# Kernel tuning notes

Hardware: AMD Instinct MI355X
Metric: run time of the kernel (lower is better)

Reference implementation:

```python
import jax, jax.numpy as jnp
import numpy as np

D_MODEL = 1024
H = 16
D_K = D_MODEL // H

def setup_inputs() -> dict:
    key = jax.random.key(0)
    ks = jax.random.split(key, 7)
    B, S = 4, 2048
    q = jax.random.normal(ks[0], (B, S, D_MODEL), dtype=jnp.float32)
    k = jax.random.normal(ks[1], (B, S, D_MODEL), dtype=jnp.float32)
    v = jax.random.normal(ks[2], (B, S, D_MODEL), dtype=jnp.float32)
    scale = 1.0 / np.sqrt(D_MODEL)
    w_q = jax.random.normal(ks[3], (D_MODEL, D_MODEL), dtype=jnp.float32) * scale
    w_k = jax.random.normal(ks[4], (D_MODEL, D_MODEL), dtype=jnp.float32) * scale
    w_v = jax.random.normal(ks[5], (D_MODEL, D_MODEL), dtype=jnp.float32) * scale
    w_o = jax.random.normal(ks[6], (D_MODEL, D_MODEL), dtype=jnp.float32) * scale
    return {"q": q, "k": k, "v": v, "w_q": w_q, "w_k": w_k, "w_v": w_v, "w_o": w_o}

def reference(q, k, v, w_q, w_k, w_v, w_o):
    B, S, _ = q.shape
    # Linear layers (no bias): x @ W^T, weights stored torch-style [out, in]
    def proj(x, w):
        y = jnp.einsum('bsd,ed->bse', x, w)
        return y.reshape(B, -1, H, D_K).transpose(0, 2, 1, 3)  # [B,H,S,d_k]
    query = proj(q, w_q)
    key_ = proj(k, w_k)
    value = proj(v, w_v)
    scores = jnp.einsum('bhqd,bhkd->bhqk', query, key_) / jnp.sqrt(jnp.float32(D_K))
    attn = jax.nn.softmax(scores, axis=-1)  # dropout p=0 -> identity
    x = jnp.einsum('bhqk,bhkd->bhqd', attn, value)
    x = x.transpose(0, 2, 1, 3).reshape(B, S, H * D_K)
    return jnp.einsum('bsd,ed->bse', x, w_o)
```

## Files before the change

### kernel.cpp

```cpp
#include <hip/hip_runtime.h>

typedef unsigned short ushort_t;
typedef __attribute__((ext_vector_type(8))) short bf16x8;
typedef __attribute__((ext_vector_type(4))) float f32x4;
typedef __attribute__((ext_vector_type(16))) float f32x16;
typedef __attribute__((ext_vector_type(4))) unsigned short ushort4v;
typedef __attribute__((ext_vector_type(4))) unsigned int uint4v;

__device__ __forceinline__ ushort_t f2bf(float f) {
  unsigned u = __float_as_uint(f);
  u += 0x7FFFu + ((u >> 16) & 1u);
  return (ushort_t)(u >> 16);
}

__device__ __forceinline__ unsigned cvt_pk(float lo, float hi) {
  unsigned r;
  asm("v_cvt_pk_bf16_f32 %0, %1, %2" : "=v"(r) : "v"(lo), "v"(hi));
  return r;
}

__device__ __forceinline__ float fast_exp2(float x) {
  float r;
  asm("v_exp_f32 %0, %1" : "=v"(r) : "v"(x));
  return r;
}

__device__ __forceinline__ void gload16(ushort_t* lds, const ushort_t* g) {
  __builtin_amdgcn_global_load_lds(
      (const __attribute__((address_space(1))) unsigned int*)g,
      (__attribute__((address_space(3))) unsigned int*)lds, 16, 0, 0);
}

__global__ void cast_w4(const float* __restrict__ s0, const float* __restrict__ s1,
                        const float* __restrict__ s2, const float* __restrict__ s3,
                        ushort_t* __restrict__ dst, int n4) {
  int i = blockIdx.x * blockDim.x + threadIdx.x;
  if (i >= n4) return;
  int z = blockIdx.y;
  const float* s = (z == 0) ? s0 : (z == 1) ? s1 : (z == 2) ? s2 : s3;
  float4 f = ((const float4*)s)[i];
  ushort4v o;
  o.x = f2bf(f.x); o.y = f2bf(f.y); o.z = f2bf(f.z); o.w = f2bf(f.w);
  ((ushort4v*)(dst + (size_t)z * n4 * 4))[i] = o;
}

template <int MODE, bool AF32>
__global__ __launch_bounds__(256, 2)
void gemm_bt(const void* __restrict__ Ap, const ushort_t* __restrict__ B,
             void* __restrict__ Cp, int M, int N, int K, float scale) {
  __shared__ __align__(16) ushort_t As[128 * 64];
  __shared__ __align__(16) ushort_t Bs[128 * 64];
  const int tid = threadIdx.x;
  const int wave = tid >> 6, lane = tid & 63;
  const int wr = wave >> 1, wc = wave & 1;
  const int frow = lane & 15, g = lane >> 4;
  const int r8 = lane >> 3, c8 = lane & 7;
  const int m0 = blockIdx.x * 128, n0 = blockIdx.y * 128;

  f32x4 acc[4][4] = {};

  const int sc = (c8 ^ r8) << 3;
  const ushort_t* Bb = B + (size_t)(n0 + wave * 32 + r8) * K + sc;
  ushort_t* AsW = &As[(wave * 32) * 64];
  ushort_t* BsW = &Bs[(wave * 32) * 64];

  const float* Af = nullptr;
  const ushort_t* Ab = nullptr;
  float a_pre[32];
  if constexpr (AF32) {
    Af = (const float*)Ap + (size_t)(m0 + wave * 32 + r8) * K + sc;
#pragma unroll
    for (int j = 0; j < 4; ++j) {
      *(float4*)&a_pre[j * 8]     = *(const float4*)(Af + (size_t)j * 8 * K);
      *(float4*)&a_pre[j * 8 + 4] = *(const float4*)(Af + (size_t)j * 8 * K + 4);
    }
  } else {
    Ab = (const ushort_t*)Ap + (size_t)(m0 + wave * 32 + r8) * K + sc;
  }

  for (int kt = 0; kt < K; kt += 64) {
    __syncthreads();
    if constexpr (AF32) {
#pragma unroll
      for (int j = 0; j < 4; ++j) {
        uint4v w;
        w[0] = cvt_pk(a_pre[j * 8 + 0], a_pre[j * 8 + 1]);
        w[1] = cvt_pk(a_pre[j * 8 + 2], a_pre[j * 8 + 3]);
        w[2] = cvt_pk(a_pre[j * 8 + 4], a_pre[j * 8 + 5]);
        w[3] = cvt_pk(a_pre[j * 8 + 6], a_pre[j * 8 + 7]);
        *(uint4v*)&AsW[j * 8 * 64 + lane * 8] = w;
        gload16(BsW + j * 8 * 64, Bb + (size_t)j * 8 * K + kt);
      }
    } else {
#pragma unroll
      for (int j = 0; j < 4; ++j) {
        gload16(AsW + j * 8 * 64, Ab + (size_t)j * 8 * K + kt);
        gload16(BsW + j * 8 * 64, Bb + (size_t)j * 8 * K + kt);
      }
    }
    __syncthreads();

    if constexpr (AF32) {
      if (kt + 64 < K) {
#pragma unroll
        for (int j = 0; j < 4; ++j) {
          *(float4*)&a_pre[j * 8]     = *(const float4*)(Af + (size_t)j * 8 * K + kt + 64);
          *(float4*)&a_pre[j * 8 + 4] = *(const float4*)(Af + (size_t)j * 8 * K + kt + 68);
        }
      }
    }

    bf16x8 af[4][2], bfr[4][2];
#pragma unroll
    for (int mi = 0; mi < 4; ++mi) {
      int row = wr * 64 + mi * 16 + frow;
#pragma unroll
      for (int ki = 0; ki < 2; ++ki)
        af[mi][ki] = *(const bf16x8*)&As[row * 64 + (((ki * 4 + g) ^ (row & 7)) << 3)];
    }
#pragma unroll
    for (int nf = 0; nf < 4; ++nf) {
      int row = wc * 64 + nf * 16 + frow;
#pragma unroll
      for (int ki = 0; ki < 2; ++ki)
        bfr[nf][ki] = *(const bf16x8*)&Bs[row * 64 + (((ki * 4 + g) ^ (row & 7)) << 3)];
    }
#pragma unroll
    for (int ki = 0; ki < 2; ++ki)
#pragma unroll
      for (int mi = 0; mi < 4; ++mi)
#pragma unroll
        for (int nf = 0; nf < 4; ++nf)
          acc[mi][nf] = __builtin_amdgcn_mfma_f32_16x16x32_bf16(
              af[mi][ki], bfr[nf][ki], acc[mi][nf], 0, 0, 0);
  }

#pragma unroll
  for (int mi = 0; mi < 4; ++mi)
#pragma unroll
    for (int nf = 0; nf < 4; ++nf)
#pragma unroll
      for (int r = 0; r < 4; ++r) {
        int m = m0 + wr * 64 + mi * 16 + g * 4 + r;
        int n = n0 + wc * 64 + nf * 16 + frow;
        float v = acc[mi][nf][r] * scale;
        if (MODE == 0) {
          ((ushort_t*)Cp)[(size_t)m * N + n] = f2bf(v);
        } else if (MODE == 1) {
          int b = m >> 11, s = m & 2047, h = n >> 6, dk = n & 63;
          ((ushort_t*)Cp)[(((size_t)((b * 16 + h) * 64 + dk)) << 11) + s] = f2bf(v);
        } else {
          ((float*)Cp)[(size_t)m * N + n] = v;
        }
      }
}

__global__ __launch_bounds__(256, 2)
void attn_kernel(const ushort_t* __restrict__ Qp, const ushort_t* __restrict__ Kp,
                 const ushort_t* __restrict__ Vt, ushort_t* __restrict__ Xb) {
  __shared__ __align__(16) ushort_t Ks[2][64 * 64];
  __shared__ __align__(16) ushort_t Vs[2][64 * 64];

  const int tid = threadIdx.x;
  const int wave = tid >> 6, lane = tid & 63;
  const int l31 = lane & 31, h = lane >> 5;
  const int f8 = lane >> 3, c8 = lane & 7;

  const int d = blockIdx.x;
  const int bh = ((d >> 6) << 3) | (d & 7);
  const int qt = (d >> 3) & 7;
  const int b = bh >> 4, hd = bh & 15;
  const int q0 = qt * 256 + wave * 64;

  bf16x8 qf[2][4];
  {
    const ushort_t* qb_ = Qp + (size_t)(b * 2048 + q0 + l31) * 1024 + hd * 64 + 8 * h;
#pragma unroll
    for (int qb = 0; qb < 2; ++qb)
#pragma unroll
      for (int ki = 0; ki < 4; ++ki)
        qf[qb][ki] = *(const bf16x8*)(qb_ + (size_t)(qb * 32) * 1024 + 16 * ki);
  }

  f32x16 oacc[2][2] = {};
  float ls[2][4] = {};

  const ushort_t* Kbase = Kp + (size_t)(b * 2048) * 1024 + hd * 64;
  const ushort_t* Vbase = Vt + ((size_t)(bh * 64) << 11);

  auto stage = [&](int kt, int sel) {
#pragma unroll
    for (int j = 0; j < 2; ++j) {
      int row = wave * 16 + j * 8 + f8;
      gload16(&Ks[sel][(wave * 16 + j * 8) * 64],
              Kbase + (size_t)(kt * 64 + row) * 1024 + ((c8 ^ f8) << 3));
      gload16(&Vs[sel][(wave * 16 + j * 8) * 64],
              Vbase + ((size_t)row << 11) + kt * 64 + ((c8 ^ f8) << 3));
    }
  };

  stage(0, 0);

  for (int kt = 0; kt < 32; ++kt) {
    const int cur = kt & 1;
    __syncthreads();
    if (kt < 31) stage(kt + 1, cur ^ 1);

    bf16x8 kf[2][4];
#pragma unroll
    for (int c = 0; c < 2; ++c)
#pragma unroll
      for (int ki = 0; ki < 4; ++ki) {
        int row = c * 32 + l31;
        kf[c][ki] = *(const bf16x8*)&Ks[cur][row * 64 + (((2 * ki + h) ^ (row & 7)) << 3)];
      }
    bf16x8 vf[4][2];
#pragma unroll
    for (int kc = 0; kc < 4; ++kc)
#pragma unroll
      for (int db = 0; db < 2; ++db) {
        int row = db * 32 + l31;
        vf[kc][db] = *(const bf16x8*)&Vs[cur][row * 64 + (((2 * kc + h) ^ (row & 7)) << 3)];
      }

#pragma unroll
    for (int qb = 0; qb < 2; ++qb) {
      f32x16 sacc[2];
      __builtin_amdgcn_s_setprio(1);
#pragma unroll
      for (int c = 0; c < 2; ++c) {
        sacc[c] = __builtin_amdgcn_mfma_f32_32x32x16_bf16(
            kf[c][0], qf[qb][0], (f32x16)(0.0f), 0, 0, 0);
#pragma unroll
        for (int ki = 1; ki < 4; ++ki)
          sacc[c] = __builtin_amdgcn_mfma_f32_32x32x16_bf16(
              kf[c][ki], qf[qb][ki], sacc[c], 0, 0, 0);
      }
      __builtin_amdgcn_s_setprio(0);

#pragma unroll
      for (int c = 0; c < 2; ++c)
#pragma unroll
        for (int r = 0; r < 16; r += 4) {
          float p0 = fast_exp2(sacc[c][r]);
          float p1 = fast_exp2(sacc[c][r + 1]);
          float p2 = fast_exp2(sacc[c][r + 2]);
          float p3 = fast_exp2(sacc[c][r + 3]);
          sacc[c][r] = p0; sacc[c][r + 1] = p1;
          sacc[c][r + 2] = p2; sacc[c][r + 3] = p3;
          ls[qb][0] += p0; ls[qb][1] += p1; ls[qb][2] += p2; ls[qb][3] += p3;
        }

      bf16x8 pfrag[4];
#pragma unroll
      for (int kc = 0; kc < 4; ++kc) {
        const int e = 2 * kc, o = 2 * kc + 1;
        const int ce = e >> 2, me = e & 3, co = o >> 2, mo = o & 3;
        unsigned x0, x1, y0, y1;
        x0 = cvt_pk(sacc[ce][4 * me],     sacc[ce][4 * me + 1]);
        x1 = cvt_pk(sacc[ce][4 * me + 2], sacc[ce][4 * me + 3]);
        y0 = cvt_pk(sacc[co][4 * mo],     sacc[co][4 * mo + 1]);
        y1 = cvt_pk(sacc[co][4 * mo + 2], sacc[co][4 * mo + 3]);
        asm("v_permlane32_swap_b32 %0, %1" : "+v"(x0), "+v"(y0));
        asm("v_permlane32_swap_b32 %0, %1" : "+v"(x1), "+v"(y1));
        uint4v pu; pu[0] = x0; pu[1] = x1; pu[2] = y0; pu[3] = y1;
        pfrag[kc] = __builtin_bit_cast(bf16x8, pu);
      }

      __builtin_amdgcn_s_setprio(1);
#pragma unroll
      for (int kc = 0; kc < 4; ++kc)
#pragma unroll
        for (int db = 0; db < 2; ++db)
          oacc[qb][db] = __builtin_amdgcn_mfma_f32_32x32x16_bf16(
              pfrag[kc], vf[kc][db], oacc[qb][db], 0, 0, 0);
      __builtin_amdgcn_s_setprio(0);
    }
  }

#pragma unroll
  for (int qb = 0; qb < 2; ++qb) {
    float lsum = (ls[qb][0] + ls[qb][1]) + (ls[qb][2] + ls[qb][3]);
    float lf = lsum + __shfl_xor(lsum, 32, 64);
    float linv = 1.0f / lf;
#pragma unroll
    for (int db = 0; db < 2; ++db)
#pragma unroll
      for (int r = 0; r < 16; ++r) {
        int qrow = (r & 3) + 8 * (r >> 2) + 4 * h;
        float li = __shfl(linv, qrow + ((db & 0) ), 64);
        int grow = b * 2048 + q0 + qb * 32 + qrow;
        int gcol = hd * 64 + db * 32 + l31;
        Xb[(size_t)grow * 1024 + gcol] = f2bf(oacc[qb][db][r] * li);
      }
  }
}

extern "C" void kernel_launch(void* const* d_in, const int* in_sizes, int n_in,
                              void* d_out, int out_size, void* d_ws, size_t ws_size,
                              hipStream_t stream) {
  const float* q = (const float*)d_in[0];
  const float* k = (const float*)d_in[1];
  const float* v = (const float*)d_in[2];
  const float* wq = (const float*)d_in[3];
  const float* wk = (const float*)d_in[4];
  const float* wv = (const float*)d_in[5];
  const float* wo = (const float*)d_in[6];

  const int M = 8192, D = 1024;
  const size_t MD = (size_t)M * D;
  const size_t DD = (size_t)D * D;

  ushort_t* ws = (ushort_t*)d_ws;
  ushort_t* buf0 = ws;
  ushort_t* Qp = buf0 + MD;
  ushort_t* Kp = Qp + MD;
  ushort_t* Vt = Kp + MD;
  ushort_t* wqb = Vt + MD;
  ushort_t* wkb = wqb + DD;
  ushort_t* wvb = wkb + DD;
  ushort_t* wob = wvb + DD;

  {
    int n4 = (int)(DD / 4);
    dim3 gw((n4 + 255) / 256, 4);
    cast_w4<<<gw, 256, 0, stream>>>(wq, wk, wv, wo, wqb, n4);
  }

  dim3 gg(M / 128, D / 128);

  gemm_bt<0, true><<<gg, 256, 0, stream>>>(q, wqb, Qp, M, D, D, 0.125f * 1.44269504f);
  gemm_bt<0, true><<<gg, 256, 0, stream>>>(k, wkb, Kp, M, D, D, 1.0f);
  gemm_bt<1, true><<<gg, 256, 0, stream>>>(v, wvb, Vt, M, D, D, 1.0f);

  attn_kernel<<<512, 256, 0, stream>>>(Qp, Kp, Vt, buf0);

  gemm_bt<2, false><<<gg, 256, 0, stream>>>(buf0, wob, (float*)d_out, M, D, D, 1.0f);
}
```

Before: 193.5 us.

## Halve per-wave query rows, double attention grid, compute row sums via MFMA

The attention kernel now gives each wave 32 query rows instead of 64, doubling the grid to 1024 blocks and raising launch bounds to 4 blocks per CU for more parallelism and occupancy. The softmax denominator is no longer summed in VALU registers; it comes from an extra MFMA of the probability fragment against a ones vector, which produces per-row sums already in the output layout and drops the shuffle-based normalization. The cost is that K/V tiles are loaded and reused by half as many query rows, doubling K/V traffic from L2, plus one extra MFMA per kc step. The row sums now use the bf16-rounded probabilities, so they match what the PV product actually multiplies by.

```diff
diff --git a/kernel.cpp b/kernel.cpp
--- a/kernel.cpp
+++ b/kernel.cpp
@@ -155,7 +155,7 @@
       }
 }
 
-__global__ __launch_bounds__(256, 2)
+__global__ __launch_bounds__(256, 4)
 void attn_kernel(const ushort_t* __restrict__ Qp, const ushort_t* __restrict__ Kp,
                  const ushort_t* __restrict__ Vt, ushort_t* __restrict__ Xb) {
   __shared__ __align__(16) ushort_t Ks[2][64 * 64];
@@ -167,23 +167,25 @@
   const int f8 = lane >> 3, c8 = lane & 7;
 
   const int d = blockIdx.x;
-  const int bh = ((d >> 6) << 3) | (d & 7);
-  const int qt = (d >> 3) & 7;
+  const int bh = ((d >> 7) << 3) | (d & 7);
+  const int qt = (d >> 3) & 15;
   const int b = bh >> 4, hd = bh & 15;
-  const int q0 = qt * 256 + wave * 64;
-
-  bf16x8 qf[2][4];
+  const int q0 = qt * 128 + wave * 32;
+
+  bf16x8 qf[4];
   {
     const ushort_t* qb_ = Qp + (size_t)(b * 2048 + q0 + l31) * 1024 + hd * 64 + 8 * h;
 #pragma unroll
-    for (int qb = 0; qb < 2; ++qb)
-#pragma unroll
-      for (int ki = 0; ki < 4; ++ki)
-        qf[qb][ki] = *(const bf16x8*)(qb_ + (size_t)(qb * 32) * 1024 + 16 * ki);
-  }
-
-  f32x16 oacc[2][2] = {};
-  float ls[2][4] = {};
+    for (int ki = 0; ki < 4; ++ki)
+      qf[ki] = *(const bf16x8*)(qb_ + 16 * ki);
+  }
+
+  const short one_bf = (short)0x3F80;
+  const bf16x8 vones = {one_bf, one_bf, one_bf, one_bf,
+                        one_bf, one_bf, one_bf, one_bf};
+
+  f32x16 oacc[2] = {};
+  f32x16 lones = {};
 
   const ushort_t* Kbase = Kp + (size_t)(b * 2048) * 1024 + hd * 64;
   const ushort_t* Vbase = Vt + ((size_t)(bh * 64) << 11);
@@ -223,77 +225,70 @@
         vf[kc][db] = *(const bf16x8*)&Vs[cur][row * 64 + (((2 * kc + h) ^ (row & 7)) << 3)];
       }
 
-#pragma unroll
-    for (int qb = 0; qb < 2; ++qb) {
-      f32x16 sacc[2];
-      __builtin_amdgcn_s_setprio(1);
-#pragma unroll
-      for (int c = 0; c < 2; ++c) {
+    f32x16 sacc[2];
+    __builtin_amdgcn_s_setprio(1);
+#pragma unroll
+    for (int c = 0; c < 2; ++c) {
+      sacc[c] = __builtin_amdgcn_mfma_f32_32x32x16_bf16(
+          kf[c][0], qf[0], (f32x16)(0.0f), 0, 0, 0);
+#pragma unroll
+      for (int ki = 1; ki < 4; ++ki)
         sacc[c] = __builtin_amdgcn_mfma_f32_32x32x16_bf16(
-            kf[c][0], qf[qb][0], (f32x16)(0.0f), 0, 0, 0);
-#pragma unroll
-        for (int ki = 1; ki < 4; ++ki)
-          sacc[c] = __builtin_amdgcn_mfma_f32_32x32x16_bf16(
-              kf[c][ki], qf[qb][ki], sacc[c], 0, 0, 0);
-      }
-      __builtin_amdgcn_s_setprio(0);
-
-#pragma unroll
-      for (int c = 0; c < 2; ++c)
-#pragma unroll
-        for (int r = 0; r < 16; r += 4) {
-          float p0 = fast_exp2(sacc[c][r]);
-          float p1 = fast_exp2(sacc[c][r + 1]);
-          float p2 = fast_exp2(sacc[c][r + 2]);
-          float p3 = fast_exp2(sacc[c][r + 3]);
-          sacc[c][r] = p0; sacc[c][r + 1] = p1;
-          sacc[c][r + 2] = p2; sacc[c][r + 3] = p3;
-          ls[qb][0] += p0; ls[qb][1] += p1; ls[qb][2] += p2; ls[qb][3] += p3;
-        }
-
-      bf16x8 pfrag[4];
-#pragma unroll
-      for (int kc = 0; kc < 4; ++kc) {
-        const int e = 2 * kc, o = 2 * kc + 1;
-        const int ce = e >> 2, me = e & 3, co = o >> 2, mo = o & 3;
-        unsigned x0, x1, y0, y1;
-        x0 = cvt_pk(sacc[ce][4 * me],     sacc[ce][4 * me + 1]);
-        x1 = cvt_pk(sacc[ce][4 * me + 2], sacc[ce][4 * me + 3]);
-        y0 = cvt_pk(sacc[co][4 * mo],     sacc[co][4 * mo + 1]);
-        y1 = cvt_pk(sacc[co][4 * mo + 2], sacc[co][4 * mo + 3]);
-        asm("v_permlane32_swap_b32 %0, %1" : "+v"(x0), "+v"(y0));
-        asm("v_permlane32_swap_b32 %0, %1" : "+v"(x1), "+v"(y1));
-        uint4v pu; pu[0] = x0; pu[1] = x1; pu[2] = y0; pu[3] = y1;
-        pfrag[kc] = __builtin_bit_cast(bf16x8, pu);
-      }
-
-      __builtin_amdgcn_s_setprio(1);
-#pragma unroll
-      for (int kc = 0; kc < 4; ++kc)
-#pragma unroll
-        for (int db = 0; db < 2; ++db)
-          oacc[qb][db] = __builtin_amdgcn_mfma_f32_32x32x16_bf16(
-              pfrag[kc], vf[kc][db], oacc[qb][db], 0, 0, 0);
-      __builtin_amdgcn_s_setprio(0);
-    }
-  }
-
-#pragma unroll
-  for (int qb = 0; qb < 2; ++qb) {
-    float lsum = (ls[qb][0] + ls[qb][1]) + (ls[qb][2] + ls[qb][3]);
-    float lf = lsum + __shfl_xor(lsum, 32, 64);
-    float linv = 1.0f / lf;
-#pragma unroll
-    for (int db = 0; db < 2; ++db)
-#pragma unroll
-      for (int r = 0; r < 16; ++r) {
-        int qrow = (r & 3) + 8 * (r >> 2) + 4 * h;
-        float li = __shfl(linv, qrow + ((db & 0) ), 64);
-        int grow = b * 2048 + q0 + qb * 32 + qrow;
-        int gcol = hd * 64 + db * 32 + l31;
-        Xb[(size_t)grow * 1024 + gcol] = f2bf(oacc[qb][db][r] * li);
-      }
-  }
+            kf[c][ki], qf[ki], sacc[c], 0, 0, 0);
+    }
+    __builtin_amdgcn_s_setprio(0);
+
+#pragma unroll
+    for (int c = 0; c < 2; ++c)
+#pragma unroll
+      for (int r = 0; r < 16; r += 4) {
+        sacc[c][r]     = fast_exp2(sacc[c][r]);
+        sacc[c][r + 1] = fast_exp2(sacc[c][r + 1]);
+        sacc[c][r + 2] = fast_exp2(sacc[c][r + 2]);
+        sacc[c][r + 3] = fast_exp2(sacc[c][r + 3]);
+      }
+
+    bf16x8 pfrag[4];
+#pragma unroll
+    for (int kc = 0; kc < 4; ++kc) {
+      const int e = 2 * kc, o = 2 * kc + 1;
+      const int ce = e >> 2, me = e & 3, co = o >> 2, mo = o & 3;
+      unsigned x0, x1, y0, y1;
+      x0 = cvt_pk(sacc[ce][4 * me],     sacc[ce][4 * me + 1]);
+      x1 = cvt_pk(sacc[ce][4 * me + 2], sacc[ce][4 * me + 3]);
+      y0 = cvt_pk(sacc[co][4 * mo],     sacc[co][4 * mo + 1]);
+      y1 = cvt_pk(sacc[co][4 * mo + 2], sacc[co][4 * mo + 3]);
+      asm("v_permlane32_swap_b32 %0, %1" : "+v"(x0), "+v"(y0));
+      asm("v_permlane32_swap_b32 %0, %1" : "+v"(x1), "+v"(y1));
+      uint4v pu; pu[0] = x0; pu[1] = x1; pu[2] = y0; pu[3] = y1;
+      pfrag[kc] = __builtin_bit_cast(bf16x8, pu);
+    }
+
+    __builtin_amdgcn_s_setprio(1);
+#pragma unroll
+    for (int kc = 0; kc < 4; ++kc) {
+      oacc[0] = __builtin_amdgcn_mfma_f32_32x32x16_bf16(
+          pfrag[kc], vf[kc][0], oacc[0], 0, 0, 0);
+      oacc[1] = __builtin_amdgcn_mfma_f32_32x32x16_bf16(
+          pfrag[kc], vf[kc][1], oacc[1], 0, 0, 0);
+      lones = __builtin_amdgcn_mfma_f32_32x32x16_bf16(
+          pfrag[kc], vones, lones, 0, 0, 0);
+    }
+    __builtin_amdgcn_s_setprio(0);
+  }
+
+  float linv[16];
+#pragma unroll
+  for (int r = 0; r < 16; ++r) linv[r] = 1.0f / lones[r];
+#pragma unroll
+  for (int db = 0; db < 2; ++db)
+#pragma unroll
+    for (int r = 0; r < 16; ++r) {
+      int qrow = (r & 3) + 8 * (r >> 2) + 4 * h;
+      int grow = b * 2048 + q0 + qrow;
+      int gcol = hd * 64 + db * 32 + l31;
+      Xb[(size_t)grow * 1024 + gcol] = f2bf(oacc[db][r] * linv[r]);
+    }
 }
 
 extern "C" void kernel_launch(void* const* d_in, const int* in_sizes, int n_in,
@@ -333,7 +328,7 @@
   gemm_bt<0, true><<<gg, 256, 0, stream>>>(k, wkb, Kp, M, D, D, 1.0f);
   gemm_bt<1, true><<<gg, 256, 0, stream>>>(v, wvb, Vt, M, D, D, 1.0f);
 
-  attn_kernel<<<512, 256, 0, stream>>>(Qp, Kp, Vt, buf0);
+  attn_kernel<<<1024, 256, 0, stream>>>(Qp, Kp, Vt, buf0);
 
   gemm_bt<2, false><<<gg, 256, 0, stream>>>(buf0, wob, (float*)d_out, M, D, D, 1.0f);
 }
```

Measured after the change: 409.4 us. 2.12x slower.
